# Optimization experiments

Hardware: AMD Instinct MI355X
Metric: run time of the kernel (lower is better)

Reference implementation:

```python
import jax, jax.numpy as jnp
import numpy as np

T, B, D, H = 512, 64, 1024, 1024  # seq_len, batch, input_dim, hidden (out_dim, bi_dir=False)


def setup_inputs() -> dict:
    key = jax.random.key(0)
    k = jax.random.split(key, 5)
    s = 1.0 / np.sqrt(H)  # PyTorch LSTMCell init scale
    x = jax.random.normal(k[0], (T, B, D), dtype=jnp.float32)
    W_ih = jax.random.uniform(k[1], (4 * H, D), minval=-s, maxval=s, dtype=jnp.float32)
    W_hh = jax.random.uniform(k[2], (4 * H, H), minval=-s, maxval=s, dtype=jnp.float32)
    b_ih = jax.random.uniform(k[3], (4 * H,), minval=-s, maxval=s, dtype=jnp.float32)
    b_hh = jax.random.uniform(k[4], (4 * H,), minval=-s, maxval=s, dtype=jnp.float32)
    return {"x": x, "W_ih": W_ih, "W_hh": W_hh, "b_ih": b_ih, "b_hh": b_hh}


def reference(x, W_ih, W_hh, b_ih, b_hh):
    # Unidirectional LSTM over [T, B, D] -> [T, B, H], PyTorch LSTMCell gate order i,f,g,o.
    # Precompute input contribution for all timesteps in one big GEMM.
    xg = jnp.einsum('tbd,gd->tbg', x, W_ih) + b_ih + b_hh  # [T, B, 4H]

    def step(carry, xg_t):
        h, c = carry
        gates = xg_t + h @ W_hh.T  # [B, 4H]
        i, f, g, o = jnp.split(gates, 4, axis=-1)
        c = jax.nn.sigmoid(f) * c + jax.nn.sigmoid(i) * jnp.tanh(g)
        h = jax.nn.sigmoid(o) * jnp.tanh(c)
        return (h, c), h

    h0 = jnp.zeros((B, H), dtype=x.dtype)
    c0 = jnp.zeros((B, H), dtype=x.dtype)
    _, hs = jax.lax.scan(step, (h0, c0), xg)  # hs: [T, B, H]
    return hs
```

## Files before the change

kernel.cpp:

```cpp
#include <hip/hip_runtime.h>
#include <hip/hip_bf16.h>
#include <stdint.h>

#define T_STEPS 512
#define BATCH   64
#define DIM     1024
#define HID     1024
#define NG      4096
#define MROWS   (T_STEPS * BATCH)

typedef __bf16 bf16;
typedef __bf16 bf16x4 __attribute__((ext_vector_type(4)));
typedef __bf16 bf16x8 __attribute__((ext_vector_type(8)));
typedef float  f32x4  __attribute__((ext_vector_type(4)));
typedef unsigned int u32;
typedef u32 u32x2 __attribute__((ext_vector_type(2)));
typedef u32 u32x4 __attribute__((ext_vector_type(4)));

__device__ __forceinline__ void g2lds16(const void* g, void* l) {
    __builtin_amdgcn_global_load_lds(
        (const __attribute__((address_space(1))) void*)g,
        (__attribute__((address_space(3))) void*)l, 16, 0, 0);
}

__device__ __forceinline__ float fsigmoid(float x) {
    return 1.0f / (1.0f + __expf(-x));
}
__device__ __forceinline__ float ftanh_(float x) {
    return 1.0f - 2.0f / (__expf(2.0f * x) + 1.0f);
}

__device__ __forceinline__ u32x4 load16_cc(const void* p) {
    u32x4 r;
    asm volatile("global_load_dwordx4 %0, %1, off sc0 sc1" : "=v"(r) : "v"(p) : "memory");
    return r;
}
__device__ __forceinline__ u32x2 load8_cached(const void* p) {
    u32x2 r;
    asm volatile("global_load_dwordx2 %0, %1, off" : "=v"(r) : "v"(p) : "memory");
    return r;
}
__device__ __forceinline__ void store2_cc(void* p, u32 v) {
    asm volatile("global_store_short %0, %1, off sc0 sc1" :: "v"(p), "v"(v) : "memory");
}
#define WAITVM(n) asm volatile("s_waitcnt vmcnt(" #n ")" ::: "memory")

__global__ __launch_bounds__(256) void prep_kernel(
    const float* __restrict__ x,   const float* __restrict__ wih,
    const float* __restrict__ bih, const float* __restrict__ bhh,
    bf16* __restrict__ xb, bf16* __restrict__ wihp,
    float* __restrict__ bsump, bf16* __restrict__ hbuf, u32* __restrict__ flags)
{
    const int nt  = gridDim.x * blockDim.x;
    const int gid = blockIdx.x * blockDim.x + threadIdx.x;

    for (int i = gid; i < MROWS * DIM / 4; i += nt) {
        f32x4 v = *(const f32x4*)(x + (size_t)i * 4);
        bf16x4 o = {(bf16)v[0], (bf16)v[1], (bf16)v[2], (bf16)v[3]};
        *(bf16x4*)(xb + (size_t)i * 4) = o;
    }
    for (int i = gid; i < NG * (DIM / 4); i += nt) {
        const int n = i >> 8, c4 = (i & 255) * 4;
        f32x4 v = *(const f32x4*)(wih + (size_t)n * DIM + c4);
        bf16x4 o = {(bf16)v[0], (bf16)v[1], (bf16)v[2], (bf16)v[3]};
        const int np = ((n & 1023) << 2) | (n >> 10);
        *(bf16x4*)(wihp + (size_t)np * DIM + c4) = o;
    }
    for (int i = gid; i < NG; i += nt)
        bsump[((i & 1023) << 2) | (i >> 10)] = bih[i] + bhh[i];
    for (int i = gid; i < BATCH * HID / 4; i += nt) {
        bf16x4 z = {(bf16)0.f, (bf16)0.f, (bf16)0.f, (bf16)0.f};
        *(bf16x4*)(hbuf + (size_t)i * 4) = z;
    }
    for (int i = gid; i < 256 * 16; i += nt)
        flags[i] = 0u;
}

__global__ __launch_bounds__(256) void gemm_kernel(
    const bf16* __restrict__ A, const bf16* __restrict__ B,
    const float* __restrict__ bsum, bf16* __restrict__ xgp)
{
    __shared__ char lds[16384];
    char* As = lds;
    char* Bs = lds + 8192;

    const int tid  = threadIdx.x;
    const int lane = tid & 63;
    const int wv   = tid >> 6;
    const int wr   = wv >> 1, wc = wv & 1;
    const int bx   = blockIdx.x & 31;
    const int by   = blockIdx.x >> 5;
    const int m0   = by * 128, n0 = bx * 128;

    f32x4 acc[4][4] = {};

    const int r4 = tid >> 2;
    const int c8 = (tid & 3) * 8;
    const size_t arow0 = (size_t)(m0 +      r4) * DIM + c8;
    const size_t arow1 = (size_t)(m0 + 64 + r4) * DIM + c8;
    const size_t brow0 = (size_t)(n0 +      r4) * DIM + c8;
    const size_t brow1 = (size_t)(n0 + 64 + r4) * DIM + c8;
    const int ldsoff = tid * 16;

    for (int k0 = 0; k0 < DIM; k0 += 32) {
        g2lds16(A + arow0 + k0, As + ldsoff);
        g2lds16(A + arow1 + k0, As + 4096 + ldsoff);
        g2lds16(B + brow0 + k0, Bs + ldsoff);
        g2lds16(B + brow1 + k0, Bs + 4096 + ldsoff);
        __syncthreads();

        bf16x8 af[4], bfr[4];
        #pragma unroll
        for (int i = 0; i < 4; ++i) {
            af[i]  = *(const bf16x8*)(As + (wr*64 + i*16 + (lane & 15))*64 + (lane >> 4)*16);
            bfr[i] = *(const bf16x8*)(Bs + (wc*64 + i*16 + (lane & 15))*64 + (lane >> 4)*16);
        }
        #pragma unroll
        for (int i = 0; i < 4; ++i)
            #pragma unroll
            for (int j = 0; j < 4; ++j)
                acc[i][j] = __builtin_amdgcn_mfma_f32_16x16x32_bf16(
                    af[i], bfr[j], acc[i][j], 0, 0, 0);
        __syncthreads();
    }

    #pragma unroll
    for (int j = 0; j < 4; ++j) {
        const int nn = n0 + wc*64 + j*16 + (lane & 15);
        const float bias = bsum[nn];
        #pragma unroll
        for (int i = 0; i < 4; ++i) {
            #pragma unroll
            for (int r = 0; r < 4; ++r) {
                const int mm = m0 + wr*64 + i*16 + ((lane >> 4) << 2) + r;
                xgp[(size_t)mm * NG + nn] = (bf16)(acc[i][j][r] + bias);
            }
        }
    }
}

__global__ __launch_bounds__(256, 1) void lstm_kernel(
    const bf16* __restrict__ xgp, const float* __restrict__ whh,
    bf16* __restrict__ hbuf, u32* __restrict__ flags, float* __restrict__ out)
{
    __shared__ short wlds[64 * 1024];
    __shared__ float gbuf[4][16][68];

    const int tid  = threadIdx.x;
    const int lane = tid & 63;
    const int wv   = tid >> 6;
    const int wg   = blockIdx.x;
    const int hg   = wg & 63;
    const int bg   = wg >> 6;

    for (int i = 0; i < 64; ++i) {
        const int grow = (i >> 4) * 1024 + hg * 16 + (i & 15);
        f32x4 v = *(const f32x4*)(whh + (size_t)grow * HID + tid * 4);
        bf16x4 o = {(bf16)v[0], (bf16)v[1], (bf16)v[2], (bf16)v[3]};
        int byte = i * 2048 + tid * 8;
        byte ^= (i & 7) << 4;
        *(bf16x4*)((char*)wlds + byte) = o;
    }

    const int frow = lane & 15;
    const int fk8  = (lane >> 4) * 8;
    const int b_el = tid >> 4;
    const int j_el = tid & 15;

    u32* myflag   = flags + ((bg * 64 + hg) << 4);
    u32* pollflag = flags + ((bg * 64 + (tid & 63)) << 4);

    float c = 0.f;
    __syncthreads();

    #pragma unroll 1
    for (int step = 0; step < T_STEPS; ++step) {
        const bf16* hb = hbuf + (step & 1) * (BATCH * HID)
                       + (size_t)(bg * 16 + frow) * HID + wv * 256 + fk8;
        u32x4 afr[8];
        #pragma unroll
        for (int kk = 0; kk < 8; ++kk)
            afr[kk] = load16_cc(hb + kk * 32);
        u32x2 xr = load8_cached(xgp + ((size_t)(step * BATCH + bg * 16 + b_el)) * NG
                                    + (16 * hg + j_el) * 4);
        WAITVM(2);
        __builtin_amdgcn_sched_barrier(0);

        f32x4 acc[4] = {};
        #pragma unroll
        for (int kk = 0; kk < 8; ++kk) {
            bf16x8 a = __builtin_bit_cast(bf16x8, afr[kk]);
            #pragma unroll
            for (int n = 0; n < 4; ++n) {
                const int row = n * 16 + frow;
                int byte = row * 2048 + wv * 512 + kk * 64 + fk8 * 2;
                byte ^= (row & 7) << 4;
                bf16x8 bfrag = *(const bf16x8*)((const char*)wlds + byte);
                acc[n] = __builtin_amdgcn_mfma_f32_16x16x32_bf16(a, bfrag, acc[n], 0, 0, 0);
            }
        }

        #pragma unroll
        for (int n = 0; n < 4; ++n)
            #pragma unroll
            for (int r = 0; r < 4; ++r)
                gbuf[wv][(lane >> 4) * 4 + r][n * 16 + frow] = acc[n][r];
        __syncthreads();

        WAITVM(0);
        __builtin_amdgcn_sched_barrier(0);
        bf16x4 xv = __builtin_bit_cast(bf16x4, xr);
        float P[4];
        #pragma unroll
        for (int g = 0; g < 4; ++g)
            P[g] = gbuf[0][b_el][g * 16 + j_el] + gbuf[1][b_el][g * 16 + j_el]
                 + gbuf[2][b_el][g * 16 + j_el] + gbuf[3][b_el][g * 16 + j_el]
                 + (float)xv[g];
        const float ig = fsigmoid(P[0]);
        const float fg = fsigmoid(P[1]);
        const float gg = ftanh_(P[2]);
        const float og = fsigmoid(P[3]);
        c = fg * c + ig * gg;
        const float hv = og * ftanh_(c);

        out[(size_t)(step * BATCH + bg * 16 + b_el) * HID + 16 * hg + j_el] = hv;
        const bf16 hb16 = (bf16)hv;
        store2_cc(hbuf + ((step & 1) ^ 1) * (BATCH * HID)
                       + (size_t)(bg * 16 + b_el) * HID + 16 * hg + j_el,
                  (u32)__builtin_bit_cast(unsigned short, hb16));

        WAITVM(0);
        __syncthreads();
        if (tid == 0)
            __hip_atomic_store(myflag, (u32)(step + 1),
                               __ATOMIC_RELAXED, __HIP_MEMORY_SCOPE_AGENT);
        while (__hip_atomic_load(pollflag, __ATOMIC_RELAXED,
                                 __HIP_MEMORY_SCOPE_AGENT) < (u32)(step + 1))
            __builtin_amdgcn_s_sleep(1);
        asm volatile("" ::: "memory");
        __syncthreads();
    }
}

extern "C" void kernel_launch(void* const* d_in, const int* in_sizes, int n_in,
                              void* d_out, int out_size, void* d_ws, size_t ws_size,
                              hipStream_t stream) {
    const float* x   = (const float*)d_in[0];
    const float* wih = (const float*)d_in[1];
    const float* whh = (const float*)d_in[2];
    const float* bih = (const float*)d_in[3];
    const float* bhh = (const float*)d_in[4];
    float* out = (float*)d_out;

    char* ws = (char*)d_ws;
    size_t off = 0;
    bf16* xgp  = (bf16*)(ws + off); off += (size_t)MROWS * NG * 2;
    bf16* xb   = (bf16*)(ws + off); off += (size_t)MROWS * DIM * 2;
    bf16* wihp = (bf16*)(ws + off); off += (size_t)NG * DIM * 2;
    float* bsum = (float*)(ws + off); off += (size_t)NG * 4;
    bf16* hbuf = (bf16*)(ws + off); off += (size_t)2 * BATCH * HID * 2;
    u32* flags = (u32*)(ws + off); off += 256 * 16 * 4;
    (void)ws_size; (void)in_sizes; (void)n_in; (void)out_size;

    prep_kernel<<<2048, 256, 0, stream>>>(x, wih, bih, bhh,
                                          xb, wihp, bsum, hbuf, flags);
    gemm_kernel<<<8192, 256, 0, stream>>>(xb, wihp, bsum, xgp);
    lstm_kernel<<<256, 256, 0, stream>>>(xgp, whh, hbuf, flags, out);
}
```

Before: 2.183 ms.

## Keep W_hh in registers, repartition LSTM blocks, and poll before step

Result: no change. 2.213 ms (+1.4%).

```diff
diff --git a/kernel.cpp b/kernel.cpp
--- a/kernel.cpp
+++ b/kernel.cpp
@@ -47,8 +47,9 @@
 
 __global__ __launch_bounds__(256) void prep_kernel(
     const float* __restrict__ x,   const float* __restrict__ wih,
-    const float* __restrict__ bih, const float* __restrict__ bhh,
-    bf16* __restrict__ xb, bf16* __restrict__ wihp,
+    const float* __restrict__ whh, const float* __restrict__ bih,
+    const float* __restrict__ bhh,
+    bf16* __restrict__ xb, bf16* __restrict__ wihp, bf16* __restrict__ wfrag,
     float* __restrict__ bsump, bf16* __restrict__ hbuf, u32* __restrict__ flags)
 {
     const int nt  = gridDim.x * blockDim.x;
@@ -65,6 +66,20 @@
         bf16x4 o = {(bf16)v[0], (bf16)v[1], (bf16)v[2], (bf16)v[3]};
         const int np = ((n & 1023) << 2) | (n >> 10);
         *(bf16x4*)(wihp + (size_t)np * DIM + c4) = o;
+    }
+    for (int i = gid; i < NG * HID / 8; i += nt) {
+        const int lane = i & 63;
+        const int f    = (i >> 6) & 63;
+        const int wv   = (i >> 12) & 3;
+        const int hg   = i >> 14;
+        const int n = f & 7, kk = f >> 3;
+        const int grow = (lane & 3) * 1024 + hg * 32 + n * 4 + ((lane & 15) >> 2);
+        const int k0   = wv * 256 + kk * 32 + (lane >> 4) * 8;
+        f32x4 v0 = *(const f32x4*)(whh + (size_t)grow * HID + k0);
+        f32x4 v1 = *(const f32x4*)(whh + (size_t)grow * HID + k0 + 4);
+        bf16x8 o = {(bf16)v0[0], (bf16)v0[1], (bf16)v0[2], (bf16)v0[3],
+                    (bf16)v1[0], (bf16)v1[1], (bf16)v1[2], (bf16)v1[3]};
+        *(bf16x8*)(wfrag + (size_t)i * 8) = o;
     }
     for (int i = gid; i < NG; i += nt)
         bsump[((i & 1023) << 2) | (i >> 10)] = bih[i] + bhh[i];
@@ -140,81 +155,79 @@
 }
 
 __global__ __launch_bounds__(256, 1) void lstm_kernel(
-    const bf16* __restrict__ xgp, const float* __restrict__ whh,
+    const bf16* __restrict__ xgp, const bf16* __restrict__ wfrag,
     bf16* __restrict__ hbuf, u32* __restrict__ flags, float* __restrict__ out)
 {
-    __shared__ short wlds[64 * 1024];
-    __shared__ float gbuf[4][16][68];
+    __shared__ float gbuf[4][8][136];
 
     const int tid  = threadIdx.x;
     const int lane = tid & 63;
     const int wv   = tid >> 6;
     const int wg   = blockIdx.x;
-    const int hg   = wg & 63;
-    const int bg   = wg >> 6;
-
-    for (int i = 0; i < 64; ++i) {
-        const int grow = (i >> 4) * 1024 + hg * 16 + (i & 15);
-        f32x4 v = *(const f32x4*)(whh + (size_t)grow * HID + tid * 4);
-        bf16x4 o = {(bf16)v[0], (bf16)v[1], (bf16)v[2], (bf16)v[3]};
-        int byte = i * 2048 + tid * 8;
-        byte ^= (i & 7) << 4;
-        *(bf16x4*)((char*)wlds + byte) = o;
-    }
-
-    const int frow = lane & 15;
-    const int fk8  = (lane >> 4) * 8;
-    const int b_el = tid >> 4;
-    const int j_el = tid & 15;
-
-    u32* myflag   = flags + ((bg * 64 + hg) << 4);
-    u32* pollflag = flags + ((bg * 64 + (tid & 63)) << 4);
+    const int hg   = wg & 31;
+    const int bg   = wg >> 5;
+
+    bf16x8 wreg[64];
+    {
+        const bf16* wb = wfrag + ((size_t)(hg * 4 + wv) * 4096 + lane) * 8;
+        #pragma unroll
+        for (int f = 0; f < 64; ++f)
+            wreg[f] = *(const bf16x8*)(wb + (size_t)f * 512);
+    }
+
+    const int frow  = lane & 15;
+    const int hrow  = bg * 8 + (frow & 7);
+    const int kbase = wv * 256 + (lane >> 4) * 8;
+    const int b_el  = tid >> 5;
+    const int j_el  = tid & 31;
+    const int hid   = hg * 32 + j_el;
+
+    const u32* pollp = flags + ((bg * 32 + wv * 8 + (lane & 7)) << 4);
+    u32* myflag      = flags + ((bg * 32 + hg) << 4);
 
     float c = 0.f;
-    __syncthreads();
+    u32x2 xr = load8_cached(xgp + (size_t)(bg * 8 + b_el) * NG + hid * 4);
 
     #pragma unroll 1
     for (int step = 0; step < T_STEPS; ++step) {
-        const bf16* hb = hbuf + (step & 1) * (BATCH * HID)
-                       + (size_t)(bg * 16 + frow) * HID + wv * 256 + fk8;
+        while (__hip_atomic_load(pollp, __ATOMIC_RELAXED,
+                                 __HIP_MEMORY_SCOPE_AGENT) < (u32)step)
+            __builtin_amdgcn_s_sleep(1);
+
+        const bf16* hb = hbuf + (step & 1) * (BATCH * HID) + (size_t)hrow * HID + kbase;
         u32x4 afr[8];
         #pragma unroll
         for (int kk = 0; kk < 8; ++kk)
             afr[kk] = load16_cc(hb + kk * 32);
-        u32x2 xr = load8_cached(xgp + ((size_t)(step * BATCH + bg * 16 + b_el)) * NG
-                                    + (16 * hg + j_el) * 4);
-        WAITVM(2);
+        WAITVM(0);
         __builtin_amdgcn_sched_barrier(0);
 
-        f32x4 acc[4] = {};
+        f32x4 acc[8] = {};
         #pragma unroll
         for (int kk = 0; kk < 8; ++kk) {
             bf16x8 a = __builtin_bit_cast(bf16x8, afr[kk]);
             #pragma unroll
-            for (int n = 0; n < 4; ++n) {
-                const int row = n * 16 + frow;
-                int byte = row * 2048 + wv * 512 + kk * 64 + fk8 * 2;
-                byte ^= (row & 7) << 4;
-                bf16x8 bfrag = *(const bf16x8*)((const char*)wlds + byte);
-                acc[n] = __builtin_amdgcn_mfma_f32_16x16x32_bf16(a, bfrag, acc[n], 0, 0, 0);
-            }
-        }
-
-        #pragma unroll
-        for (int n = 0; n < 4; ++n)
-            #pragma unroll
-            for (int r = 0; r < 4; ++r)
-                gbuf[wv][(lane >> 4) * 4 + r][n * 16 + frow] = acc[n][r];
-        __syncthreads();
-
-        WAITVM(0);
-        __builtin_amdgcn_sched_barrier(0);
+            for (int n = 0; n < 8; ++n)
+                acc[n] = __builtin_amdgcn_mfma_f32_16x16x32_bf16(
+                    a, wreg[kk * 8 + n], acc[n], 0, 0, 0);
+        }
+
+        if (lane < 32) {
+            const int q = lane >> 4;
+            #pragma unroll
+            for (int n = 0; n < 8; ++n)
+                #pragma unroll
+                for (int r = 0; r < 4; ++r)
+                    gbuf[wv][q * 4 + r][n * 16 + frow] = acc[n][r];
+        }
+        __syncthreads();
+
         bf16x4 xv = __builtin_bit_cast(bf16x4, xr);
         float P[4];
         #pragma unroll
         for (int g = 0; g < 4; ++g)
-            P[g] = gbuf[0][b_el][g * 16 + j_el] + gbuf[1][b_el][g * 16 + j_el]
-                 + gbuf[2][b_el][g * 16 + j_el] + gbuf[3][b_el][g * 16 + j_el]
+            P[g] = gbuf[0][b_el][j_el * 4 + g] + gbuf[1][b_el][j_el * 4 + g]
+                 + gbuf[2][b_el][j_el * 4 + g] + gbuf[3][b_el][j_el * 4 + g]
                  + (float)xv[g];
         const float ig = fsigmoid(P[0]);
         const float fg = fsigmoid(P[1]);
@@ -223,22 +236,20 @@
         c = fg * c + ig * gg;
         const float hv = og * ftanh_(c);
 
-        out[(size_t)(step * BATCH + bg * 16 + b_el) * HID + 16 * hg + j_el] = hv;
-        const bf16 hb16 = (bf16)hv;
+        const bf16 h16 = (bf16)hv;
         store2_cc(hbuf + ((step & 1) ^ 1) * (BATCH * HID)
-                       + (size_t)(bg * 16 + b_el) * HID + 16 * hg + j_el,
-                  (u32)__builtin_bit_cast(unsigned short, hb16));
-
+                       + (size_t)(bg * 8 + b_el) * HID + hid,
+                  (u32)__builtin_bit_cast(unsigned short, h16));
         WAITVM(0);
         __syncthreads();
         if (tid == 0)
             __hip_atomic_store(myflag, (u32)(step + 1),
                                __ATOMIC_RELAXED, __HIP_MEMORY_SCOPE_AGENT);
-        while (__hip_atomic_load(pollflag, __ATOMIC_RELAXED,
-                                 __HIP_MEMORY_SCOPE_AGENT) < (u32)(step + 1))
-            __builtin_amdgcn_s_sleep(1);
-        asm volatile("" ::: "memory");
-        __syncthreads();
+
+        out[(size_t)(step * BATCH + bg * 8 + b_el) * HID + hid] = hv;
+        if (step + 1 < T_STEPS)
+            xr = load8_cached(xgp + ((size_t)((step + 1) * BATCH) + bg * 8 + b_el) * NG
+                                  + hid * 4);
     }
 }
 
@@ -254,16 +265,17 @@
 
     char* ws = (char*)d_ws;
     size_t off = 0;
-    bf16* xgp  = (bf16*)(ws + off); off += (size_t)MROWS * NG * 2;
-    bf16* xb   = (bf16*)(ws + off); off += (size_t)MROWS * DIM * 2;
-    bf16* wihp = (bf16*)(ws + off); off += (size_t)NG * DIM * 2;
+    bf16* xgp   = (bf16*)(ws + off); off += (size_t)MROWS * NG * 2;
+    bf16* xb    = (bf16*)(ws + off); off += (size_t)MROWS * DIM * 2;
+    bf16* wihp  = (bf16*)(ws + off); off += (size_t)NG * DIM * 2;
+    bf16* wfrag = (bf16*)(ws + off); off += (size_t)NG * HID * 2;
     float* bsum = (float*)(ws + off); off += (size_t)NG * 4;
-    bf16* hbuf = (bf16*)(ws + off); off += (size_t)2 * BATCH * HID * 2;
-    u32* flags = (u32*)(ws + off); off += 256 * 16 * 4;
+    bf16* hbuf  = (bf16*)(ws + off); off += (size_t)2 * BATCH * HID * 2;
+    u32* flags  = (u32*)(ws + off); off += 256 * 16 * 4;
     (void)ws_size; (void)in_sizes; (void)n_in; (void)out_size;
 
-    prep_kernel<<<2048, 256, 0, stream>>>(x, wih, bih, bhh,
-                                          xb, wihp, bsum, hbuf, flags);
+    prep_kernel<<<2048, 256, 0, stream>>>(x, wih, whh, bih, bhh,
+                                          xb, wihp, wfrag, bsum, hbuf, flags);
     gemm_kernel<<<8192, 256, 0, stream>>>(xb, wihp, bsum, xgp);
-    lstm_kernel<<<256, 256, 0, stream>>>(xgp, whh, hbuf, flags, out);
-}
+    lstm_kernel<<<256, 256, 0, stream>>>(xgp, wfrag, hbuf, flags, out);
+}
```
